# Kernel optimization log

Measured on AMD Instinct MI355X. Metric: run time of the kernel, lower is better.

Reference implementation:

```python
import jax, jax.numpy as jnp
import numpy as np

EMBED = 1024
HEADS = 16
HEAD_DIM = EMBED // HEADS


def setup_inputs() -> dict:
    key = jax.random.key(0)
    ks = jax.random.split(key, 11)
    B, S, D = 2, 2048, EMBED
    scale = 1.0 / np.sqrt(D)
    inp = {
        "q": jax.random.normal(ks[0], (B, S, D), jnp.float32),
        "k": jax.random.normal(ks[1], (B, S, D), jnp.float32),
        "v": jax.random.normal(ks[2], (B, S, D), jnp.float32),
        "Wq": jax.random.normal(ks[3], (D, D), jnp.float32) * scale,
        "bq": jnp.zeros((D,), jnp.float32),
        "Wk": jax.random.normal(ks[4], (D, D), jnp.float32) * scale,
        "bk": jnp.zeros((D,), jnp.float32),
        "Wv": jax.random.normal(ks[5], (D, D), jnp.float32) * scale,
        "bv": jnp.zeros((D,), jnp.float32),
        "Wo": jax.random.normal(ks[6], (D, D), jnp.float32) * scale,
        "bo": jnp.zeros((D,), jnp.float32),
    }
    return inp


def _split_heads(x):
    b, n, c = x.shape
    return x.reshape(b, n, HEADS, c // HEADS).transpose(0, 2, 1, 3)  # [b,h,n,dh]


def reference(q, k, v, Wq, bq, Wk, bk, Wv, bv, Wo, bo):
    qh = _split_heads(q @ Wq + bq)
    kh = _split_heads(k @ Wk + bk)
    vh = _split_heads(v @ Wv + bv)
    scale = 1.0 / jnp.sqrt(jnp.asarray(HEAD_DIM, qh.dtype))
    att = jnp.einsum("bhqd,bhkd->bhqk", qh, kh) * scale
    att = jax.nn.softmax(att, axis=-1)
    out = jnp.einsum("bhqk,bhkd->bhqd", att, vh)
    b, h, n, dh = out.shape
    out = out.transpose(0, 2, 1, 3).reshape(b, n, h * dh)
    return out @ Wo + bo
```

## Files before the change

### kernel.cpp

```cpp
#include <hip/hip_runtime.h>
#include <hip/hip_bf16.h>
#include <stdint.h>

typedef unsigned short u16;
typedef __bf16 bf16x8 __attribute__((ext_vector_type(8)));
typedef float f32x4 __attribute__((ext_vector_type(4)));
typedef float f32x16 __attribute__((ext_vector_type(16)));
typedef unsigned int u32x4 __attribute__((ext_vector_type(4)));
typedef unsigned int u32x2 __attribute__((ext_vector_type(2)));

#define S_LEN 2048
#define DMODEL 1024
#define NHEAD 16
#define DHEAD 64
#define MROWS 4096
#define EXP2SCALE 0.180336880112f

__device__ __forceinline__ u16 f2b(float f) {
  __hip_bfloat16 h = __float2bfloat16(f);
  union { __hip_bfloat16 h; u16 u; } c;
  c.h = h;
  return c.u;
}
__device__ __forceinline__ unsigned int pk2(float lo, float hi) {
  return (unsigned int)f2b(lo) | ((unsigned int)f2b(hi) << 16);
}
__device__ __forceinline__ unsigned int cvtpk(float a, float b) {
  unsigned int r;
  asm("v_cvt_pk_bf16_f32 %0, %1, %2" : "=v"(r) : "v"(a), "v"(b));
  return r;
}
__device__ __forceinline__ void plswap(unsigned int &a, unsigned int &b) {
  auto r = __builtin_amdgcn_permlane32_swap((int)a, (int)b, false, false);
  a = (unsigned int)r[0];
  b = (unsigned int)r[1];
}

__device__ __forceinline__ void gload16(const void* g, void* l) {
  __builtin_amdgcn_global_load_lds(
      (const __attribute__((address_space(1))) unsigned int*)(uintptr_t)g,
      (__attribute__((address_space(3))) unsigned int*)(uintptr_t)l,
      16, 0, 0);
}

__global__ __launch_bounds__(256) void prep(
    const float* __restrict__ q, const float* __restrict__ k, const float* __restrict__ v,
    const float* __restrict__ Wq, const float* __restrict__ Wk,
    const float* __restrict__ Wv, const float* __restrict__ Wo,
    u16* __restrict__ Qx, u16* __restrict__ Kx, u16* __restrict__ Vx,
    u16* __restrict__ Wqt, u16* __restrict__ Wkt,
    u16* __restrict__ Wvt, u16* __restrict__ Wot) {
  __shared__ u16 tile[64][65];
  const int z = blockIdx.z;
  const int tid = threadIdx.x;
  if (z < 3) {
    const float* src = (z == 0) ? q : (z == 1) ? k : v;
    u16* dst = (z == 0) ? Qx : (z == 1) ? Kx : Vx;
    const size_t i8 = ((size_t)blockIdx.x * 256 + tid) * 8;
    float4 a = *(const float4*)(src + i8);
    float4 b = *(const float4*)(src + i8 + 4);
    u16 o[8];
    o[0] = f2b(a.x); o[1] = f2b(a.y); o[2] = f2b(a.z); o[3] = f2b(a.w);
    o[4] = f2b(b.x); o[5] = f2b(b.y); o[6] = f2b(b.z); o[7] = f2b(b.w);
    *(u32x4*)(dst + i8) = *(const u32x4*)o;
    return;
  }
  if (blockIdx.x >= 256) return;
  const int zz = z - 3;
  const float* W = (zz == 0) ? Wq : (zz == 1) ? Wk : (zz == 2) ? Wv : Wo;
  u16* Wt = (zz == 0) ? Wqt : (zz == 1) ? Wkt : (zz == 2) ? Wvt : Wot;
  const int n0 = (blockIdx.x & 15) * 64, k0 = (blockIdx.x >> 4) * 64;
#pragma unroll
  for (int j = 0; j < 16; j++) {
    int idx = j * 256 + tid;
    int r = idx >> 6, c = idx & 63;
    tile[r][c] = f2b(W[(size_t)(k0 + r) * DMODEL + n0 + c]);
  }
  __syncthreads();
#pragma unroll
  for (int j = 0; j < 16; j++) {
    int idx = j * 256 + tid;
    int r = idx >> 6, c = idx & 63;
    Wt[(size_t)(n0 + r) * DMODEL + k0 + c] = tile[c][r];
  }
}

template <int MODE>
__device__ __forceinline__ void gemm_body(const u16* __restrict__ A,
                                          const u16* __restrict__ Bt,
                                          const float* __restrict__ bias,
                                          void* __restrict__ Cv,
                                          u16* __restrict__ As,
                                          u16* __restrict__ Bs) {
  constexpr int K = DMODEL;
  const int tid = threadIdx.x;
  const int wave = tid >> 6, lane = tid & 63;
  const int quad = lane >> 4, l15 = lane & 15;
  const int wr = wave >> 1, wc = wave & 1;
  const int lid = blockIdx.y * 8 + blockIdx.x;
  const int sw = (lid & 7) * 32 + (lid >> 3);
  const int bcol = sw & 7, brow = sw >> 3;

  f32x4 acc[4][4] = {};

  for (int k0 = 0; k0 < K; k0 += 64) {
    __syncthreads();
#pragma unroll
    for (int t = 0; t < 4; t++) {
      const int slot = t * 256 + wave * 64 + lane;
      const int row = slot >> 3;
      const int cgc = ((slot & 7) ^ (row & 7)) << 3;
      const int ldsb = (t * 256 + wave * 64) * 8;
      gload16(A + (size_t)(brow * 128 + row) * K + k0 + cgc, As + ldsb);
      gload16(Bt + (size_t)(bcol * 128 + row) * K + k0 + cgc, Bs + ldsb);
    }
    __syncthreads();

#pragma unroll
    for (int kk = 0; kk < 2; kk++) {
      bf16x8 af[4], bfm[4];
#pragma unroll
      for (int i = 0; i < 4; i++)
        af[i] = *(const bf16x8*)(As + (wr * 64 + i * 16 + l15) * 64 +
                                 ((((kk << 2) + quad) ^ (l15 & 7)) << 3));
#pragma unroll
      for (int j = 0; j < 4; j++)
        bfm[j] = *(const bf16x8*)(Bs + (wc * 64 + j * 16 + l15) * 64 +
                                  ((((kk << 2) + quad) ^ (l15 & 7)) << 3));
#pragma unroll
      for (int i = 0; i < 4; i++)
#pragma unroll
        for (int j = 0; j < 4; j++)
          acc[i][j] = __builtin_amdgcn_mfma_f32_16x16x32_bf16(af[i], bfm[j], acc[i][j], 0, 0, 0);
    }
  }

#pragma unroll
  for (int i = 0; i < 4; i++)
#pragma unroll
    for (int j = 0; j < 4; j++) {
      const int col = bcol * 128 + wc * 64 + j * 16 + l15;
      const float bv = bias[col];
      if (MODE == 2) {
        const int srow = brow * 128 + wr * 64 + i * 16 + quad * 4;
        const int bb = srow >> 11, s = srow & (S_LEN - 1);
        u32x2 pd;
        pd.x = pk2(acc[i][j][0] + bv, acc[i][j][1] + bv);
        pd.y = pk2(acc[i][j][2] + bv, acc[i][j][3] + bv);
        *(u32x2*)((u16*)Cv + ((size_t)(bb * 1024 + col)) * S_LEN + s) = pd;
      } else {
#pragma unroll
        for (int r = 0; r < 4; r++) {
          const int row = brow * 128 + wr * 64 + i * 16 + quad * 4 + r;
          if (MODE == 1)
            ((float*)Cv)[(size_t)row * DMODEL + col] = acc[i][j][r] + bv;
          else if (MODE == 3)
            ((u16*)Cv)[(size_t)row * DMODEL + col] = f2b((acc[i][j][r] + bv) * EXP2SCALE);
          else
            ((u16*)Cv)[(size_t)row * DMODEL + col] = f2b(acc[i][j][r] + bv);
        }
      }
    }
}

__global__ __launch_bounds__(256, 4) void gemm_qkv(
    const u16* __restrict__ Qx, const u16* __restrict__ Kx, const u16* __restrict__ Vx,
    const u16* __restrict__ Wqt, const u16* __restrict__ Wkt, const u16* __restrict__ Wvt,
    const float* __restrict__ bq, const float* __restrict__ bk, const float* __restrict__ bv,
    u16* __restrict__ Qp, u16* __restrict__ Kp, u16* __restrict__ Vt) {
  __shared__ u16 As[128 * 64];
  __shared__ u16 Bs[128 * 64];
  const int z = blockIdx.z;
  if (z == 2) {
    gemm_body<2>(Vx, Wvt, bv, Vt, As, Bs);
  } else if (z == 0) {
    gemm_body<3>(Qx, Wqt, bq, Qp, As, Bs);
  } else {
    gemm_body<0>(Kx, Wkt, bk, Kp, As, Bs);
  }
}

__global__ __launch_bounds__(256, 4) void gemm_out(
    const u16* __restrict__ A, const u16* __restrict__ Bt,
    const float* __restrict__ bias, float* __restrict__ C) {
  __shared__ u16 As[128 * 64];
  __shared__ u16 Bs[128 * 64];
  gemm_body<1>(A, Bt, bias, C, As, Bs);
}

#define ISSUE_KV(ksb, vsb)              \
  do {                                  \
    gload16(pK0, (ksb) + dstu);         \
    gload16(pK1, (ksb) + 2048 + dstu);  \
    gload16(pV0, (vsb) + dstu);         \
    gload16(pV1, (vsb) + 2048 + dstu);  \
    pK0 += 64 * DMODEL; pK1 += 64 * DMODEL; \
    pV0 += 64; pV1 += 64;               \
  } while (0)

#define TILE_COMPUTE(ksb, vsb)                                                     \
  do {                                                                             \
    f32x16 sA = {}, sB = {};                                                       \
    __builtin_amdgcn_s_setprio(1);                                                 \
    _Pragma("unroll") for (int c = 0; c < 4; c++) {                                \
      bf16x8 ka0 = *(const bf16x8*)((ksb) + off[c]);                               \
      bf16x8 ka1 = *(const bf16x8*)((ksb) + off[c] + 2048);                        \
      sA = __builtin_amdgcn_mfma_f32_32x32x16_bf16(ka0, qf[c], sA, 0, 0, 0);       \
      sB = __builtin_amdgcn_mfma_f32_32x32x16_bf16(ka1, qf[c], sB, 0, 0, 0);       \
    }                                                                              \
    __builtin_amdgcn_s_setprio(0);                                                 \
    bf16x8 pf[4];                                                                  \
    _Pragma("unroll") for (int kb = 0; kb < 2; kb++) {                             \
      const f32x16 s = kb ? sB : sA;                                               \
      unsigned int cc[8];                                                          \
      _Pragma("unroll") for (int m = 0; m < 8; m++)                                \
        cc[m] = cvtpk(__builtin_amdgcn_exp2f(s[2 * m]),                            \
                      __builtin_amdgcn_exp2f(s[2 * m + 1]));                       \
      plswap(cc[0], cc[2]);                                                        \
      plswap(cc[1], cc[3]);                                                        \
      plswap(cc[4], cc[6]);                                                        \
      plswap(cc[5], cc[7]);                                                        \
      union { unsigned int u[4]; bf16x8 v; } f0, f1;                               \
      f0.u[0] = cc[0]; f0.u[1] = cc[1]; f0.u[2] = cc[2]; f0.u[3] = cc[3];          \
      f1.u[0] = cc[4]; f1.u[1] = cc[5]; f1.u[2] = cc[6]; f1.u[3] = cc[7];          \
      pf[2 * kb] = f0.v; pf[2 * kb + 1] = f1.v;                                    \
    }                                                                              \
    __builtin_amdgcn_s_setprio(1);                                                 \
    _Pragma("unroll") for (int g = 0; g < 4; g++) {                                \
      bf16x8 v0 = *(const bf16x8*)((vsb) + off[g]);                                \
      bf16x8 v1 = *(const bf16x8*)((vsb) + off[g] + 2048);                         \
      lacc  = __builtin_amdgcn_mfma_f32_32x32x16_bf16(pf[g], ones, lacc, 0, 0, 0); \
      oacc0 = __builtin_amdgcn_mfma_f32_32x32x16_bf16(pf[g], v0, oacc0, 0, 0, 0);  \
      oacc1 = __builtin_amdgcn_mfma_f32_32x32x16_bf16(pf[g], v1, oacc1, 0, 0, 0);  \
    }                                                                              \
    __builtin_amdgcn_s_setprio(0);                                                 \
  } while (0)

__global__ __launch_bounds__(256) void attn(const u16* __restrict__ Qp,
                                            const u16* __restrict__ Kp,
                                            const u16* __restrict__ Vt,
                                            u16* __restrict__ Op) {
  __shared__ u16 Ks0[64 * 64], Ks1[64 * 64];
  __shared__ u16 Vs0[64 * 64], Vs1[64 * 64];

  const int tid = threadIdx.x;
  const int wave = tid >> 6, lane = tid & 63;
  const int row31 = lane & 31, hl = lane >> 5;

  const int id = blockIdx.x + (blockIdx.y << 4) + (blockIdx.z << 8);
  const int sw = ((id & 7) << 6) + (id >> 3);
  const int qt = sw & 15, h = (sw >> 4) & 15, b = sw >> 8;
  const int s0 = qt * 128;

  const size_t baseK = ((size_t)(b * S_LEN)) * DMODEL + h * DHEAD;
  const size_t baseV = ((size_t)((b * NHEAD + h) * DHEAD)) * S_LEN;

  const int r0 = tid >> 3;
  const int cg = (tid & 7) ^ (r0 & 7);
  const u16* pK0 = Kp + baseK + (size_t)r0 * DMODEL + cg * 8;
  const u16* pK1 = pK0 + (size_t)32 * DMODEL;
  const u16* pV0 = Vt + baseV + (size_t)r0 * S_LEN + cg * 8;
  const u16* pV1 = pV0 + (size_t)32 * S_LEN;
  const int dstu = wave * 512;

  int off[4];
#pragma unroll
  for (int c = 0; c < 4; c++)
    off[c] = row31 * 64 + ((((c << 1) + hl) ^ (row31 & 7)) << 3);

  bf16x8 ones;
  {
    union { u16 a[8]; bf16x8 v; } c;
#pragma unroll
    for (int j = 0; j < 8; j++) c.a[j] = 0x3F80;
    ones = c.v;
  }

  bf16x8 qf[4];
#pragma unroll
  for (int c = 0; c < 4; c++)
    qf[c] = *(const bf16x8*)(Qp +
        ((size_t)(b * S_LEN + s0 + wave * 32 + row31)) * DMODEL +
        h * DHEAD + c * 16 + hl * 8);

  f32x16 oacc0 = {}, oacc1 = {};
  f32x16 lacc = {};

  ISSUE_KV(Ks0, Vs0);

#pragma unroll 1
  for (int kt = 0; kt < 32; kt += 2) {
    __syncthreads();
    ISSUE_KV(Ks1, Vs1);
    TILE_COMPUTE(Ks0, Vs0);
    __syncthreads();
    if (kt + 2 < 32) ISSUE_KV(Ks0, Vs0);
    TILE_COMPUTE(Ks1, Vs1);
  }

#pragma unroll
  for (int r = 0; r < 16; r++) {
    const float inv = 1.0f / lacc[r];
    const int qrow = (r & 3) + 8 * (r >> 2) + 4 * hl;
    const size_t rb = ((size_t)(b * S_LEN + s0 + wave * 32 + qrow)) * DMODEL + h * DHEAD;
    Op[rb + row31]      = f2b(oacc0[r] * inv);
    Op[rb + 32 + row31] = f2b(oacc1[r] * inv);
  }
}

extern "C" void kernel_launch(void* const* d_in, const int* in_sizes, int n_in,
                              void* d_out, int out_size, void* d_ws, size_t ws_size,
                              hipStream_t stream) {
  const float* q  = (const float*)d_in[0];
  const float* k  = (const float*)d_in[1];
  const float* v  = (const float*)d_in[2];
  const float* Wq = (const float*)d_in[3];
  const float* bq = (const float*)d_in[4];
  const float* Wk = (const float*)d_in[5];
  const float* bk = (const float*)d_in[6];
  const float* Wv = (const float*)d_in[7];
  const float* bv = (const float*)d_in[8];
  const float* Wo = (const float*)d_in[9];
  const float* bo = (const float*)d_in[10];

  char* w = (char*)d_ws;
  const size_t WSZ = (size_t)DMODEL * DMODEL * 2;
  const size_t XSZ = (size_t)MROWS * DMODEL * 2;
  u16* Wqt = (u16*)(w);
  u16* Wkt = (u16*)(w + WSZ);
  u16* Wvt = (u16*)(w + 2 * WSZ);
  u16* Wot = (u16*)(w + 3 * WSZ);
  u16* Qx  = (u16*)(w + 4 * WSZ);
  u16* Kx  = (u16*)(w + 4 * WSZ + XSZ);
  u16* Vx  = (u16*)(w + 4 * WSZ + 2 * XSZ);
  u16* Qp  = (u16*)(w + 4 * WSZ + 3 * XSZ);
  u16* Kp  = (u16*)(w + 4 * WSZ + 4 * XSZ);
  u16* Vt  = (u16*)(w + 4 * WSZ + 5 * XSZ);
  u16* Op  = (u16*)(w + 4 * WSZ + 6 * XSZ);

  prep<<<dim3(2048, 1, 7), 256, 0, stream>>>(q, k, v, Wq, Wk, Wv, Wo,
                                             Qx, Kx, Vx, Wqt, Wkt, Wvt, Wot);
  gemm_qkv<<<dim3(8, 32, 3), 256, 0, stream>>>(Qx, Kx, Vx, Wqt, Wkt, Wvt,
                                               bq, bk, bv, Qp, Kp, Vt);
  attn<<<dim3(16, 16, 2), 256, 0, stream>>>(Qp, Kp, Vt, Op);
  gemm_out<<<dim3(8, 32, 1), 256, 0, stream>>>(Op, Wot, bo, (float*)d_out);
}
```

Measured before the change: 209.5 us.

## Fuse activation bf16 conversion into QKV GEMM and split attention keys across wave groups

```diff
diff --git a/kernel.cpp b/kernel.cpp
--- a/kernel.cpp
+++ b/kernel.cpp
@@ -44,29 +44,13 @@
 }
 
 __global__ __launch_bounds__(256) void prep(
-    const float* __restrict__ q, const float* __restrict__ k, const float* __restrict__ v,
     const float* __restrict__ Wq, const float* __restrict__ Wk,
     const float* __restrict__ Wv, const float* __restrict__ Wo,
-    u16* __restrict__ Qx, u16* __restrict__ Kx, u16* __restrict__ Vx,
     u16* __restrict__ Wqt, u16* __restrict__ Wkt,
     u16* __restrict__ Wvt, u16* __restrict__ Wot) {
   __shared__ u16 tile[64][65];
-  const int z = blockIdx.z;
+  const int zz = blockIdx.z;
   const int tid = threadIdx.x;
-  if (z < 3) {
-    const float* src = (z == 0) ? q : (z == 1) ? k : v;
-    u16* dst = (z == 0) ? Qx : (z == 1) ? Kx : Vx;
-    const size_t i8 = ((size_t)blockIdx.x * 256 + tid) * 8;
-    float4 a = *(const float4*)(src + i8);
-    float4 b = *(const float4*)(src + i8 + 4);
-    u16 o[8];
-    o[0] = f2b(a.x); o[1] = f2b(a.y); o[2] = f2b(a.z); o[3] = f2b(a.w);
-    o[4] = f2b(b.x); o[5] = f2b(b.y); o[6] = f2b(b.z); o[7] = f2b(b.w);
-    *(u32x4*)(dst + i8) = *(const u32x4*)o;
-    return;
-  }
-  if (blockIdx.x >= 256) return;
-  const int zz = z - 3;
   const float* W = (zz == 0) ? Wq : (zz == 1) ? Wk : (zz == 2) ? Wv : Wo;
   u16* Wt = (zz == 0) ? Wqt : (zz == 1) ? Wkt : (zz == 2) ? Wvt : Wot;
   const int n0 = (blockIdx.x & 15) * 64, k0 = (blockIdx.x >> 4) * 64;
@@ -85,14 +69,16 @@
   }
 }
 
-template <int MODE>
-__device__ __forceinline__ void gemm_body(const u16* __restrict__ A,
+template <int MODE, int AF32>
+__device__ __forceinline__ void gemm_body(const void* __restrict__ Av,
                                           const u16* __restrict__ Bt,
                                           const float* __restrict__ bias,
                                           void* __restrict__ Cv,
                                           u16* __restrict__ As,
                                           u16* __restrict__ Bs) {
   constexpr int K = DMODEL;
+  const float* Af = (const float*)Av;
+  const u16* Ab = (const u16*)Av;
   const int tid = threadIdx.x;
   const int wave = tid >> 6, lane = tid & 63;
   const int quad = lane >> 4, l15 = lane & 15;
@@ -102,19 +88,55 @@
   const int bcol = sw & 7, brow = sw >> 3;
 
   f32x4 acc[4][4] = {};
+  float4 ar[8];
+
+  if (AF32) {
+#pragma unroll
+    for (int j = 0; j < 8; j++)
+      ar[j] = *(const float4*)(Af +
+          (size_t)(brow * 128 + j * 16 + (tid >> 4)) * DMODEL + ((tid & 15) * 4));
+  }
 
   for (int k0 = 0; k0 < K; k0 += 64) {
     __syncthreads();
-#pragma unroll
-    for (int t = 0; t < 4; t++) {
-      const int slot = t * 256 + wave * 64 + lane;
-      const int row = slot >> 3;
-      const int cgc = ((slot & 7) ^ (row & 7)) << 3;
-      const int ldsb = (t * 256 + wave * 64) * 8;
-      gload16(A + (size_t)(brow * 128 + row) * K + k0 + cgc, As + ldsb);
-      gload16(Bt + (size_t)(bcol * 128 + row) * K + k0 + cgc, Bs + ldsb);
+    if (AF32) {
+#pragma unroll
+      for (int j = 0; j < 8; j++) {
+        const int r = j * 16 + (tid >> 4);
+        const int c = (tid & 15) >> 1;
+        u32x2 wv;
+        wv.x = cvtpk(ar[j].x, ar[j].y);
+        wv.y = cvtpk(ar[j].z, ar[j].w);
+        *(u32x2*)(As + r * 64 + ((c ^ (r & 7)) << 3) + (tid & 1) * 4) = wv;
+      }
+#pragma unroll
+      for (int t = 0; t < 4; t++) {
+        const int slot = t * 256 + wave * 64 + lane;
+        const int row = slot >> 3;
+        const int cgc = ((slot & 7) ^ (row & 7)) << 3;
+        const int ldsb = (t * 256 + wave * 64) * 8;
+        gload16(Bt + (size_t)(bcol * 128 + row) * K + k0 + cgc, Bs + ldsb);
+      }
+    } else {
+#pragma unroll
+      for (int t = 0; t < 4; t++) {
+        const int slot = t * 256 + wave * 64 + lane;
+        const int row = slot >> 3;
+        const int cgc = ((slot & 7) ^ (row & 7)) << 3;
+        const int ldsb = (t * 256 + wave * 64) * 8;
+        gload16(Ab + (size_t)(brow * 128 + row) * K + k0 + cgc, As + ldsb);
+        gload16(Bt + (size_t)(bcol * 128 + row) * K + k0 + cgc, Bs + ldsb);
+      }
     }
     __syncthreads();
+
+    if (AF32 && k0 + 64 < K) {
+#pragma unroll
+      for (int j = 0; j < 8; j++)
+        ar[j] = *(const float4*)(Af +
+            (size_t)(brow * 128 + j * 16 + (tid >> 4)) * DMODEL +
+            (k0 + 64) + ((tid & 15) * 4));
+    }
 
 #pragma unroll
     for (int kk = 0; kk < 2; kk++) {
@@ -163,8 +185,8 @@
     }
 }
 
-__global__ __launch_bounds__(256, 4) void gemm_qkv(
-    const u16* __restrict__ Qx, const u16* __restrict__ Kx, const u16* __restrict__ Vx,
+__global__ __launch_bounds__(256, 3) void gemm_qkv(
+    const float* __restrict__ q, const float* __restrict__ k, const float* __restrict__ v,
     const u16* __restrict__ Wqt, const u16* __restrict__ Wkt, const u16* __restrict__ Wvt,
     const float* __restrict__ bq, const float* __restrict__ bk, const float* __restrict__ bv,
     u16* __restrict__ Qp, u16* __restrict__ Kp, u16* __restrict__ Vt) {
@@ -172,11 +194,11 @@
   __shared__ u16 Bs[128 * 64];
   const int z = blockIdx.z;
   if (z == 2) {
-    gemm_body<2>(Vx, Wvt, bv, Vt, As, Bs);
+    gemm_body<2, 1>(v, Wvt, bv, Vt, As, Bs);
   } else if (z == 0) {
-    gemm_body<3>(Qx, Wqt, bq, Qp, As, Bs);
+    gemm_body<3, 1>(q, Wqt, bq, Qp, As, Bs);
   } else {
-    gemm_body<0>(Kx, Wkt, bk, Kp, As, Bs);
+    gemm_body<0, 1>(k, Wkt, bk, Kp, As, Bs);
   }
 }
 
@@ -185,18 +207,8 @@
     const float* __restrict__ bias, float* __restrict__ C) {
   __shared__ u16 As[128 * 64];
   __shared__ u16 Bs[128 * 64];
-  gemm_body<1>(A, Bt, bias, C, As, Bs);
-}
-
-#define ISSUE_KV(ksb, vsb)              \
-  do {                                  \
-    gload16(pK0, (ksb) + dstu);         \
-    gload16(pK1, (ksb) + 2048 + dstu);  \
-    gload16(pV0, (vsb) + dstu);         \
-    gload16(pV1, (vsb) + 2048 + dstu);  \
-    pK0 += 64 * DMODEL; pK1 += 64 * DMODEL; \
-    pV0 += 64; pV1 += 64;               \
-  } while (0)
+  gemm_body<1, 0>(A, Bt, bias, C, As, Bs);
+}
 
 #define TILE_COMPUTE(ksb, vsb)                                                     \
   do {                                                                             \
@@ -236,16 +248,29 @@
     __builtin_amdgcn_s_setprio(0);                                                 \
   } while (0)
 
-__global__ __launch_bounds__(256) void attn(const u16* __restrict__ Qp,
-                                            const u16* __restrict__ Kp,
-                                            const u16* __restrict__ Vt,
-                                            u16* __restrict__ Op) {
-  __shared__ u16 Ks0[64 * 64], Ks1[64 * 64];
-  __shared__ u16 Vs0[64 * 64], Vs1[64 * 64];
+#define ISSUE(buf, kt)                                                            \
+  do {                                                                            \
+    if (wave < 4) {                                                               \
+      const u16* g = srcK + (size_t)(kt) * 64 * DMODEL;                           \
+      _Pragma("unroll") for (int j = 0; j < 4; j++)                               \
+        gload16(g + (size_t)j * 8 * DMODEL, dst0 + (buf) * 4096 + j * 512);       \
+    } else {                                                                      \
+      const u16* g = srcV + (kt) * 64;                                            \
+      _Pragma("unroll") for (int j = 0; j < 4; j++)                               \
+        gload16(g + (size_t)j * 8 * S_LEN, dst0 + (buf) * 4096 + j * 512);        \
+    }                                                                             \
+  } while (0)
+
+__global__ __launch_bounds__(512, 4) void attn(const u16* __restrict__ Qp,
+                                               const u16* __restrict__ Kp,
+                                               const u16* __restrict__ Vt,
+                                               u16* __restrict__ Op) {
+  __shared__ u16 LB[32768];
 
   const int tid = threadIdx.x;
   const int wave = tid >> 6, lane = tid & 63;
   const int row31 = lane & 31, hl = lane >> 5;
+  const int qg = wave & 3, kh = wave >> 2;
 
   const int id = blockIdx.x + (blockIdx.y << 4) + (blockIdx.z << 8);
   const int sw = ((id & 7) << 6) + (id >> 3);
@@ -255,13 +280,15 @@
   const size_t baseK = ((size_t)(b * S_LEN)) * DMODEL + h * DHEAD;
   const size_t baseV = ((size_t)((b * NHEAD + h) * DHEAD)) * S_LEN;
 
-  const int r0 = tid >> 3;
-  const int cg = (tid & 7) ^ (r0 & 7);
-  const u16* pK0 = Kp + baseK + (size_t)r0 * DMODEL + cg * 8;
-  const u16* pK1 = pK0 + (size_t)32 * DMODEL;
-  const u16* pV0 = Vt + baseV + (size_t)r0 * S_LEN + cg * 8;
-  const u16* pV1 = pV0 + (size_t)32 * S_LEN;
-  const int dstu = wave * 512;
+  const int sub = wave & 1, khd = (wave >> 1) & 1;
+  const int rl = lane >> 3, cl = lane & 7;
+  const int cg8 = (cl ^ rl) << 3;
+  const u16* srcK = Kp + baseK + (size_t)(khd * 1024 + sub * 32 + rl) * DMODEL + cg8;
+  const u16* srcV = Vt + baseV + (size_t)(sub * 32 + rl) * S_LEN + khd * 1024 + cg8;
+  u16* dst0 = LB + (wave >= 4 ? 16384 : 0) + khd * 8192 + (sub * 32) * 64;
+
+  const u16* kcb = LB + kh * 8192;
+  const u16* vcb = LB + 16384 + kh * 8192;
 
   int off[4];
 #pragma unroll
@@ -280,31 +307,47 @@
 #pragma unroll
   for (int c = 0; c < 4; c++)
     qf[c] = *(const bf16x8*)(Qp +
-        ((size_t)(b * S_LEN + s0 + wave * 32 + row31)) * DMODEL +
+        ((size_t)(b * S_LEN + s0 + qg * 32 + row31)) * DMODEL +
         h * DHEAD + c * 16 + hl * 8);
 
   f32x16 oacc0 = {}, oacc1 = {};
   f32x16 lacc = {};
 
-  ISSUE_KV(Ks0, Vs0);
+  ISSUE(0, 0);
 
 #pragma unroll 1
-  for (int kt = 0; kt < 32; kt += 2) {
+  for (int kt = 0; kt < 16; kt += 2) {
     __syncthreads();
-    ISSUE_KV(Ks1, Vs1);
-    TILE_COMPUTE(Ks0, Vs0);
+    ISSUE(1, kt + 1);
+    TILE_COMPUTE(kcb, vcb);
     __syncthreads();
-    if (kt + 2 < 32) ISSUE_KV(Ks0, Vs0);
-    TILE_COMPUTE(Ks1, Vs1);
-  }
-
-#pragma unroll
-  for (int r = 0; r < 16; r++) {
-    const float inv = 1.0f / lacc[r];
-    const int qrow = (r & 3) + 8 * (r >> 2) + 4 * hl;
-    const size_t rb = ((size_t)(b * S_LEN + s0 + wave * 32 + qrow)) * DMODEL + h * DHEAD;
-    Op[rb + row31]      = f2b(oacc0[r] * inv);
-    Op[rb + 32 + row31] = f2b(oacc1[r] * inv);
+    if (kt + 2 < 16) ISSUE(0, kt + 2);
+    TILE_COMPUTE(kcb + 4096, vcb + 4096);
+  }
+
+  __syncthreads();
+  float* M = ((float*)LB) + qg * 3072;
+  if (kh == 1) {
+#pragma unroll
+    for (int r = 0; r < 16; r++) {
+      M[r * 64 + lane]        = oacc0[r];
+      M[1024 + r * 64 + lane] = oacc1[r];
+      M[2048 + r * 64 + lane] = lacc[r];
+    }
+  }
+  __syncthreads();
+  if (kh == 0) {
+#pragma unroll
+    for (int r = 0; r < 16; r++) {
+      const float o0 = oacc0[r] + M[r * 64 + lane];
+      const float o1 = oacc1[r] + M[1024 + r * 64 + lane];
+      const float ls = lacc[r] + M[2048 + r * 64 + lane];
+      const float inv = 1.0f / ls;
+      const int qrow = (r & 3) + 8 * (r >> 2) + 4 * hl;
+      const size_t rb = ((size_t)(b * S_LEN + s0 + qg * 32 + qrow)) * DMODEL + h * DHEAD;
+      Op[rb + row31]      = f2b(o0 * inv);
+      Op[rb + 32 + row31] = f2b(o1 * inv);
+    }
   }
 }
 
@@ -330,18 +373,14 @@
   u16* Wkt = (u16*)(w + WSZ);
   u16* Wvt = (u16*)(w + 2 * WSZ);
   u16* Wot = (u16*)(w + 3 * WSZ);
-  u16* Qx  = (u16*)(w + 4 * WSZ);
-  u16* Kx  = (u16*)(w + 4 * WSZ + XSZ);
-  u16* Vx  = (u16*)(w + 4 * WSZ + 2 * XSZ);
-  u16* Qp  = (u16*)(w + 4 * WSZ + 3 * XSZ);
-  u16* Kp  = (u16*)(w + 4 * WSZ + 4 * XSZ);
-  u16* Vt  = (u16*)(w + 4 * WSZ + 5 * XSZ);
-  u16* Op  = (u16*)(w + 4 * WSZ + 6 * XSZ);
-
-  prep<<<dim3(2048, 1, 7), 256, 0, stream>>>(q, k, v, Wq, Wk, Wv, Wo,
-                                             Qx, Kx, Vx, Wqt, Wkt, Wvt, Wot);
-  gemm_qkv<<<dim3(8, 32, 3), 256, 0, stream>>>(Qx, Kx, Vx, Wqt, Wkt, Wvt,
+  u16* Qp  = (u16*)(w + 4 * WSZ);
+  u16* Kp  = (u16*)(w + 4 * WSZ + XSZ);
+  u16* Vt  = (u16*)(w + 4 * WSZ + 2 * XSZ);
+  u16* Op  = (u16*)(w + 4 * WSZ + 3 * XSZ);
+
+  prep<<<dim3(256, 1, 4), 256, 0, stream>>>(Wq, Wk, Wv, Wo, Wqt, Wkt, Wvt, Wot);
+  gemm_qkv<<<dim3(8, 32, 3), 256, 0, stream>>>(q, k, v, Wqt, Wkt, Wvt,
                                                bq, bk, bv, Qp, Kp, Vt);
-  attn<<<dim3(16, 16, 2), 256, 0, stream>>>(Qp, Kp, Vt, Op);
+  attn<<<dim3(16, 16, 2), 512, 0, stream>>>(Qp, Kp, Vt, Op);
   gemm_out<<<dim3(8, 32, 1), 256, 0, stream>>>(Op, Wot, bo, (float*)d_out);
 }
```

Measured after the change: 212.5 us. About the same (+1.4%).
